# Optimization experiments

Measured on AMD Instinct MI355X. Metric: run time of the kernel, lower is better.

The kernel has to match this reference:

```python
import jax, jax.numpy as jnp
import numpy as np

QUERY_DIM = 768
KEY_DIM = 1024


def setup_inputs() -> dict:
    key = jax.random.key(0)
    ks = jax.random.split(key, 8)
    B, LQ, LK = 16, 2048, 2048
    s_q = 1.0 / np.sqrt(QUERY_DIM)
    s_k = 1.0 / np.sqrt(KEY_DIM)
    return {
        "query": jax.random.normal(ks[0], (B, LQ, QUERY_DIM), jnp.float32),
        "key": jax.random.normal(ks[1], (B, LK, KEY_DIM), jnp.float32),
        "Wq": jax.random.uniform(ks[2], (QUERY_DIM, KEY_DIM), jnp.float32, -s_q, s_q),
        "bq": jax.random.uniform(ks[3], (KEY_DIM,), jnp.float32, -s_q, s_q),
        "Wk": jax.random.uniform(ks[4], (KEY_DIM, KEY_DIM), jnp.float32, -s_k, s_k),
        "bk": jax.random.uniform(ks[5], (KEY_DIM,), jnp.float32, -s_k, s_k),
        "Wv": jax.random.uniform(ks[6], (KEY_DIM, KEY_DIM), jnp.float32, -s_k, s_k),
        "bv": jax.random.uniform(ks[7], (KEY_DIM,), jnp.float32, -s_k, s_k),
    }


def reference(query, key, Wq, bq, Wk, bk, Wv, bv):
    # Linear projections (single-head)
    q = jnp.einsum('bqd,dk->bqk', query, Wq) + bq  # [B, Lq, Dk]
    k = jnp.einsum('bsd,dk->bsk', key, Wk) + bk    # [B, Lk, Dk]
    v = jnp.einsum('bsd,dk->bsk', key, Wv) + bv    # [B, Lk, Dk]
    d_k = k.shape[-1]
    scores = jnp.einsum('bqk,bsk->bqs', q, k) / jnp.sqrt(jnp.asarray(d_k, q.dtype))
    weights = jax.nn.softmax(scores, axis=-1)      # [B, Lq, Lk]
    return jnp.einsum('bqs,bsk->bqk', weights, v)  # [B, Lq, Dk]
```

## Files before the change

kernel.cpp:

```cpp
#include <hip/hip_runtime.h>
#include <hip/hip_bf16.h>


typedef __attribute__((ext_vector_type(4))) float  f32x4;
typedef __attribute__((ext_vector_type(8))) __bf16 bf16x8;

#define BM 256
#define BN 256
#define BK 32

__device__ __forceinline__ void gload_lds16(const __bf16* g, __bf16* l) {
    __builtin_amdgcn_global_load_lds(
        (const __attribute__((address_space(1))) void*)g,
        (__attribute__((address_space(3))) void*)l, 16, 0, 0);
}

enum { MODE_PROJ = 0, MODE_PROJT = 1, MODE_SCORE = 2, MODE_PV = 3 };

#define MF(m_, a_)                                                              \
    acc[m_][0] = __builtin_amdgcn_mfma_f32_16x16x32_bf16(a_, b0, acc[m_][0], 0, 0, 0); \
    acc[m_][1] = __builtin_amdgcn_mfma_f32_16x16x32_bf16(a_, b1, acc[m_][1], 0, 0, 0); \
    acc[m_][2] = __builtin_amdgcn_mfma_f32_16x16x32_bf16(a_, b2, acc[m_][2], 0, 0, 0); \
    acc[m_][3] = __builtin_amdgcn_mfma_f32_16x16x32_bf16(a_, b3, acc[m_][3], 0, 0, 0);

#define TILE_STEP(CA_, CB_, SA_, SB_, DO_STAGE, VM_WAIT) do {                   \
    bf16x8 a0, a1, a2, a3, a4, a5, a6, a7, b0, b1, b2, b3;                      \
                                        \
    b0 = *(const bf16x8*)&CB_[raB];                                             \
    b1 = *(const bf16x8*)&CB_[raB + 512];                                       \
    b2 = *(const bf16x8*)&CB_[raB + 1024];                                      \
    b3 = *(const bf16x8*)&CB_[raB + 1536];                                      \
    a0 = *(const bf16x8*)&CA_[raA];                                             \
    a1 = *(const bf16x8*)&CA_[raA + 512];                                       \
    a2 = *(const bf16x8*)&CA_[raA + 1024];                                      \
    a3 = *(const bf16x8*)&CA_[raA + 1536];                                      \
    if (DO_STAGE) {                                                             \
        gload_lds16(ap0, &SA_[wA]);                                             \
        gload_lds16(ap1, &SA_[wA + 512]);                                       \
        ap0 += BK; ap1 += BK;                                                   \
    }                                                                           \
    __builtin_amdgcn_s_barrier();                                               \
    __builtin_amdgcn_s_setprio(1);                                              \
    MF(0, a0) MF(1, a1) MF(2, a2) MF(3, a3)                                     \
    __builtin_amdgcn_s_setprio(0);                                              \
    __builtin_amdgcn_s_barrier();                                               \
                        \
    a4 = *(const bf16x8*)&CA_[raA + 2048];                                      \
    a5 = *(const bf16x8*)&CA_[raA + 2560];                                      \
    a6 = *(const bf16x8*)&CA_[raA + 3072];                                      \
    a7 = *(const bf16x8*)&CA_[raA + 3584];                                      \
    if (DO_STAGE) {                                                             \
        gload_lds16(bp0, &SB_[wA]);                                             \
        gload_lds16(bp1, &SB_[wA + 512]);                                       \
        bp0 += BK; bp1 += BK;                                                   \
    }                                                                           \
    VM_WAIT;                                                                    \
    __builtin_amdgcn_s_barrier();                                               \
    __builtin_amdgcn_s_setprio(1);                                              \
    MF(4, a4) MF(5, a5) MF(6, a6) MF(7, a7)                                     \
    __builtin_amdgcn_s_setprio(0);                                              \
    __builtin_amdgcn_s_barrier();                                               \
} while (0)

template <int MODE>
__global__ __launch_bounds__(512, 2) void gemm256(
    const __bf16* __restrict__ Ag, const __bf16* __restrict__ Bg,
    const float* __restrict__ aux,
    float* __restrict__ rs,
    void* __restrict__ Cg,
    int K, int lda, int ldb, int ldc,
    long batchA, long batchB, long batchC, long batchRS)
{
    __shared__ __bf16 As0[BM * BK], As1[BM * BK], As2[BM * BK], As3[BM * BK];
    __shared__ __bf16 Bs0[BN * BK], Bs1[BN * BK], Bs2[BN * BK], Bs3[BN * BK];
    const int t    = threadIdx.x;
    const int lane = t & 63;
    const int w    = t >> 6;
    const int quad = lane >> 4;
    const int l15  = lane & 15;
    const int wm   = w >> 2, wn = w & 3;
    const int m0   = blockIdx.x * BM;
    const int n0   = blockIdx.y * BN;
    const int z    = blockIdx.z;

    const __bf16* A = Ag + (long)z * batchA;
    const __bf16* B = Bg + (long)z * batchB;

    const int srow = lane >> 2;
    const int sq   = ((lane & 3) ^ ((lane >> 3) & 3)) * 8;
    const __bf16* ap0 = A + (long)(m0 + w * 32 +      srow) * lda + sq;
    const __bf16* ap1 = A + (long)(m0 + w * 32 + 16 + srow) * lda + sq;
    const __bf16* bp0 = B + (long)(n0 + w * 32 +      srow) * ldb + sq;
    const __bf16* bp1 = B + (long)(n0 + w * 32 + 16 + srow) * ldb + sq;
    const int wA = w * 1024;

    const int swz = (quad ^ ((l15 >> 1) & 3)) * 8;
    const int raA = (wm * 128 + l15) * BK + swz;
    const int raB = (wn * 64  + l15) * BK + swz;

    f32x4 acc[8][4];
    #pragma unroll
    for (int i = 0; i < 8; ++i)
        #pragma unroll
        for (int j = 0; j < 4; ++j) acc[i][j] = (f32x4)(0.0f);

    const int NT = K / BK;

    gload_lds16(ap0, &As0[wA]); gload_lds16(ap1, &As0[wA + 512]);
    gload_lds16(bp0, &Bs0[wA]); gload_lds16(bp1, &Bs0[wA + 512]);
    ap0 += BK; ap1 += BK; bp0 += BK; bp1 += BK;
    gload_lds16(ap0, &As1[wA]); gload_lds16(ap1, &As1[wA + 512]);
    gload_lds16(bp0, &Bs1[wA]); gload_lds16(bp1, &Bs1[wA + 512]);
    ap0 += BK; ap1 += BK; bp0 += BK; bp1 += BK;
    gload_lds16(ap0, &As2[wA]); gload_lds16(ap1, &As2[wA + 512]);
    gload_lds16(bp0, &Bs2[wA]); gload_lds16(bp1, &Bs2[wA + 512]);
    ap0 += BK; ap1 += BK; bp0 += BK; bp1 += BK;
    asm volatile("s_waitcnt vmcnt(8)");
    __builtin_amdgcn_s_barrier();

    const int chunks = (NT - 4) >> 2;
    for (int c = 0; c < chunks; ++c) {
        TILE_STEP(As0, Bs0, As3, Bs3, 1, asm volatile("s_waitcnt vmcnt(8)"));
        TILE_STEP(As1, Bs1, As0, Bs0, 1, asm volatile("s_waitcnt vmcnt(8)"));
        TILE_STEP(As2, Bs2, As1, Bs1, 1, asm volatile("s_waitcnt vmcnt(8)"));
        TILE_STEP(As3, Bs3, As2, Bs2, 1, asm volatile("s_waitcnt vmcnt(8)"));
    }
    TILE_STEP(As0, Bs0, As3, Bs3, 1, asm volatile("s_waitcnt vmcnt(8)"));
    TILE_STEP(As1, Bs1, As0, Bs0, 0, asm volatile("s_waitcnt vmcnt(4)"));
    TILE_STEP(As2, Bs2, As0, Bs0, 0, asm volatile("s_waitcnt vmcnt(0)"));
    TILE_STEP(As3, Bs3, As0, Bs0, 0, ((void)0));

    const int rowbase = m0 + wm * 128;
    const int colbase = n0 + wn * 64;

    if constexpr (MODE == MODE_PROJ) {
        __bf16* C = (__bf16*)Cg;
        #pragma unroll
        for (int n = 0; n < 4; ++n) {
            const int col = colbase + n * 16 + l15;
            const float bv = aux[col];
            #pragma unroll
            for (int m = 0; m < 8; ++m)
                #pragma unroll
                for (int r = 0; r < 4; ++r) {
                    const int row = rowbase + m * 16 + quad * 4 + r;
                    C[(long)row * ldc + col] = (__bf16)(acc[m][n][r] + bv);
                }
        }
    } else if constexpr (MODE == MODE_PROJT) {
        __bf16* C = (__bf16*)Cg;
        #pragma unroll
        for (int m = 0; m < 8; ++m)
            #pragma unroll
            for (int r = 0; r < 4; ++r) {
                const int row = rowbase + m * 16 + quad * 4 + r;
                const float bv = aux[row];
                #pragma unroll
                for (int n = 0; n < 4; ++n) {
                    const int col = colbase + n * 16 + l15;
                    const long idx = (long)(col >> 11) * (1024L * 2048)
                                   + (long)row * 2048 + (col & 2047);
                    C[idx] = (__bf16)(acc[m][n][r] + bv);
                }
            }
    } else if constexpr (MODE == MODE_SCORE) {
        const float sc = 0.03125f * 1.44269504088896f;
        __bf16* C = (__bf16*)Cg + (long)z * batchC;
        float* rsz = rs + (long)z * batchRS;
        #pragma unroll
        for (int m = 0; m < 8; ++m) {
            float s[4] = {0.f, 0.f, 0.f, 0.f};
            #pragma unroll
            for (int n = 0; n < 4; ++n) {
                const int col = colbase + n * 16 + l15;
                #pragma unroll
                for (int r = 0; r < 4; ++r) {
                    const int row = rowbase + m * 16 + quad * 4 + r;
                    const float e = exp2f(acc[m][n][r] * sc);
                    C[(long)row * ldc + col] = (__bf16)e;
                    s[r] += e;
                }
            }
            #pragma unroll
            for (int r = 0; r < 4; ++r) {
                float v = s[r];
                v += __shfl_xor(v, 1);
                v += __shfl_xor(v, 2);
                v += __shfl_xor(v, 4);
                v += __shfl_xor(v, 8);
                if (l15 == 0)
                    atomicAdd(&rsz[rowbase + m * 16 + quad * 4 + r], v);
            }
        }
    } else {
        float* C = (float*)Cg + (long)z * batchC;
        const float* rsz = rs + (long)z * batchRS;
        #pragma unroll
        for (int m = 0; m < 8; ++m) {
            float inv[4];
            #pragma unroll
            for (int r = 0; r < 4; ++r)
                inv[r] = 1.0f / rsz[rowbase + m * 16 + quad * 4 + r];
            #pragma unroll
            for (int n = 0; n < 4; ++n) {
                const int col = colbase + n * 16 + l15;
                #pragma unroll
                for (int r = 0; r < 4; ++r) {
                    const int row = rowbase + m * 16 + quad * 4 + r;
                    C[(long)row * ldc + col] = acc[m][n][r] * inv[r];
                }
            }
        }
    }
}

__global__ __launch_bounds__(256) void conv_bf16(const float* __restrict__ in,
                                                 __bf16* __restrict__ out, long n8)
{
    const long stride = (long)gridDim.x * blockDim.x;
    for (long i = (long)blockIdx.x * blockDim.x + threadIdx.x; i < n8; i += stride) {
        const float4* p = (const float4*)(in + i * 8);
        const float4 a = p[0], b = p[1];
        bf16x8 o;
        o[0] = (__bf16)a.x; o[1] = (__bf16)a.y; o[2] = (__bf16)a.z; o[3] = (__bf16)a.w;
        o[4] = (__bf16)b.x; o[5] = (__bf16)b.y; o[6] = (__bf16)b.z; o[7] = (__bf16)b.w;
        *(bf16x8*)(out + i * 8) = o;
    }
}

__global__ __launch_bounds__(256) void transpose_w(const float* __restrict__ W,
                                                   __bf16* __restrict__ WT,
                                                   int K, int N)
{
    __shared__ float tile[32][33];
    const int n0 = blockIdx.x * 32, k0 = blockIdx.y * 32;
    const int c = threadIdx.x & 31, r4 = threadIdx.x >> 5;
    #pragma unroll
    for (int i = 0; i < 4; ++i) {
        const int r = r4 + i * 8;
        tile[r][c] = W[(long)(k0 + r) * N + n0 + c];
    }
    __syncthreads();
    #pragma unroll
    for (int i = 0; i < 4; ++i) {
        const int r = r4 + i * 8;
        WT[(long)(n0 + r) * K + k0 + c] = (__bf16)tile[c][r];
    }
}

extern "C" void kernel_launch(void* const* d_in, const int* in_sizes, int n_in,
                              void* d_out, int out_size, void* d_ws, size_t ws_size,
                              hipStream_t stream) {
    const float* query = (const float*)d_in[0];
    const float* key   = (const float*)d_in[1];
    const float* Wq    = (const float*)d_in[2];
    const float* bq    = (const float*)d_in[3];
    const float* Wk    = (const float*)d_in[4];
    const float* bk    = (const float*)d_in[5];
    const float* Wv    = (const float*)d_in[6];
    const float* bv    = (const float*)d_in[7];
    float* out = (float*)d_out;

    const int B = 16, Lq = 2048, Lk = 2048, Dq = 768, Dk = 1024;
    const long M = (long)B * Lq;

    char* base = (char*)d_ws;
    __bf16* P   = (__bf16*)base;
    __bf16* qa  = (__bf16*)base;
    __bf16* ka  = (__bf16*)(base + 50331648);
    __bf16* WqT = (__bf16*)(base + 117440512);
    __bf16* WkT = (__bf16*)(base + 119013376);
    __bf16* WvT = (__bf16*)(base + 121110528);
    char* p2 = base + 134217728;
    __bf16* q  = (__bf16*)p2;  p2 += M * Dk * 2;
    __bf16* k  = (__bf16*)p2;  p2 += M * Dk * 2;
    __bf16* vT = (__bf16*)p2;  p2 += M * Dk * 2;
    float* row_sum = (float*)p2; p2 += M * 4;
    if ((size_t)(p2 - base) > ws_size) return;

    dim3 blk(256);
    dim3 blk5(512);

    conv_bf16<<<512, blk, 0, stream>>>(query, qa, M * Dq / 8);
    conv_bf16<<<512, blk, 0, stream>>>(key,   ka, M * Dk / 8);
    transpose_w<<<dim3(Dk / 32, Dq / 32), blk, 0, stream>>>(Wq, WqT, Dq, Dk);
    transpose_w<<<dim3(Dk / 32, Dk / 32), blk, 0, stream>>>(Wk, WkT, Dk, Dk);
    transpose_w<<<dim3(Dk / 32, Dk / 32), blk, 0, stream>>>(Wv, WvT, Dk, Dk);
    hipMemsetAsync(row_sum, 0, M * 4, stream);

    gemm256<MODE_PROJ><<<dim3(M / BM, Dk / BN, 1), blk5, 0, stream>>>(
        qa, WqT, bq, nullptr, q, Dq, Dq, Dq, Dk, 0, 0, 0, 0);
    gemm256<MODE_PROJ><<<dim3(M / BM, Dk / BN, 1), blk5, 0, stream>>>(
        ka, WkT, bk, nullptr, k, Dk, Dk, Dk, Dk, 0, 0, 0, 0);
    gemm256<MODE_PROJT><<<dim3(Dk / BM, M / BN, 1), blk5, 0, stream>>>(
        WvT, ka, bv, nullptr, vT, Dk, Dk, Dk, 0, 0, 0, 0, 0);

    gemm256<MODE_SCORE><<<dim3(Lq / BM, Lk / BN, B), blk5, 0, stream>>>(
        q, k, nullptr, row_sum, P, Dk, Dk, Dk, Lk,
        (long)Lq * Dk, (long)Lk * Dk, (long)Lq * Lk, Lq);

    gemm256<MODE_PV><<<dim3(Lq / BM, Dk / BN, B), blk5, 0, stream>>>(
        P, vT, nullptr, row_sum, out, Lk, Lk, 2048, Dk,
        (long)Lq * Lk, 1024L * 2048, (long)Lq * Dk, Lq);
}
```

Measured before the change: 914.7 us.

## Replace direct global-to-LDS loads with register-staged double buffering

Global tiles are now loaded into registers one step ahead and written to LDS with ordinary vector stores, replacing the four-stage global_load_lds pipeline with a two-buffer LDS ping-pong. This cuts shared memory from four stages to two per operand, which could allow more resident blocks or lower LDS pressure. In exchange it costs extra VGPRs for the staged data and adds LDS write traffic and lgkmcnt waits inside the main loop, and it shortens the prefetch distance.

```diff
diff --git a/kernel.cpp b/kernel.cpp
--- a/kernel.cpp
+++ b/kernel.cpp
@@ -8,12 +8,6 @@
 #define BM 256
 #define BN 256
 #define BK 32
-
-__device__ __forceinline__ void gload_lds16(const __bf16* g, __bf16* l) {
-    __builtin_amdgcn_global_load_lds(
-        (const __attribute__((address_space(1))) void*)g,
-        (__attribute__((address_space(3))) void*)l, 16, 0, 0);
-}
 
 enum { MODE_PROJ = 0, MODE_PROJT = 1, MODE_SCORE = 2, MODE_PV = 3 };
 
@@ -23,9 +17,15 @@
     acc[m_][2] = __builtin_amdgcn_mfma_f32_16x16x32_bf16(a_, b2, acc[m_][2], 0, 0, 0); \
     acc[m_][3] = __builtin_amdgcn_mfma_f32_16x16x32_bf16(a_, b3, acc[m_][3], 0, 0, 0);
 
-#define TILE_STEP(CA_, CB_, SA_, SB_, DO_STAGE, VM_WAIT) do {                   \
+#define TILE_STEP(CA_, CB_, WA_, WB_, w0_, w1_, w2_, w3_,                       \
+                  l0_, l1_, l2_, l3_, DO_WRITE, DO_LOAD) do {                   \
     bf16x8 a0, a1, a2, a3, a4, a5, a6, a7, b0, b1, b2, b3;                      \
-                                        \
+     \
+    if (DO_LOAD) {                                                              \
+        l0_ = *(const bf16x8*)ap0; l1_ = *(const bf16x8*)ap1;                   \
+        l2_ = *(const bf16x8*)bp0; l3_ = *(const bf16x8*)bp1;                   \
+        ap0 += BK; ap1 += BK; bp0 += BK; bp1 += BK;                             \
+    }                                                                           \
     b0 = *(const bf16x8*)&CB_[raB];                                             \
     b1 = *(const bf16x8*)&CB_[raB + 512];                                       \
     b2 = *(const bf16x8*)&CB_[raB + 1024];                                      \
@@ -34,27 +34,23 @@
     a1 = *(const bf16x8*)&CA_[raA + 512];                                       \
     a2 = *(const bf16x8*)&CA_[raA + 1024];                                      \
     a3 = *(const bf16x8*)&CA_[raA + 1536];                                      \
-    if (DO_STAGE) {                                                             \
-        gload_lds16(ap0, &SA_[wA]);                                             \
-        gload_lds16(ap1, &SA_[wA + 512]);                                       \
-        ap0 += BK; ap1 += BK;                                                   \
+    if (DO_WRITE) {               \
+        *(bf16x8*)&WA_[wA + lane8]       = w0_;                                 \
+        *(bf16x8*)&WA_[wA + 512 + lane8] = w1_;                                 \
+        *(bf16x8*)&WB_[wA + lane8]       = w2_;                                 \
+        *(bf16x8*)&WB_[wA + 512 + lane8] = w3_;                                 \
     }                                                                           \
     __builtin_amdgcn_s_barrier();                                               \
     __builtin_amdgcn_s_setprio(1);                                              \
     MF(0, a0) MF(1, a1) MF(2, a2) MF(3, a3)                                     \
     __builtin_amdgcn_s_setprio(0);                                              \
+    if (DO_WRITE) asm volatile("s_waitcnt lgkmcnt(0)");     \
     __builtin_amdgcn_s_barrier();                                               \
-                        \
+                                                         \
     a4 = *(const bf16x8*)&CA_[raA + 2048];                                      \
     a5 = *(const bf16x8*)&CA_[raA + 2560];                                      \
     a6 = *(const bf16x8*)&CA_[raA + 3072];                                      \
     a7 = *(const bf16x8*)&CA_[raA + 3584];                                      \
-    if (DO_STAGE) {                                                             \
-        gload_lds16(bp0, &SB_[wA]);                                             \
-        gload_lds16(bp1, &SB_[wA + 512]);                                       \
-        bp0 += BK; bp1 += BK;                                                   \
-    }                                                                           \
-    VM_WAIT;                                                                    \
     __builtin_amdgcn_s_barrier();                                               \
     __builtin_amdgcn_s_setprio(1);                                              \
     MF(4, a4) MF(5, a5) MF(6, a6) MF(7, a7)                                     \
@@ -71,8 +67,8 @@
     int K, int lda, int ldb, int ldc,
     long batchA, long batchB, long batchC, long batchRS)
 {
-    __shared__ __bf16 As0[BM * BK], As1[BM * BK], As2[BM * BK], As3[BM * BK];
-    __shared__ __bf16 Bs0[BN * BK], Bs1[BN * BK], Bs2[BN * BK], Bs3[BN * BK];
+    __shared__ __bf16 As0[BM * BK], As1[BM * BK];
+    __shared__ __bf16 Bs0[BN * BK], Bs1[BN * BK];
     const int t    = threadIdx.x;
     const int lane = t & 63;
     const int w    = t >> 6;
@@ -92,7 +88,8 @@
     const __bf16* ap1 = A + (long)(m0 + w * 32 + 16 + srow) * lda + sq;
     const __bf16* bp0 = B + (long)(n0 + w * 32 +      srow) * ldb + sq;
     const __bf16* bp1 = B + (long)(n0 + w * 32 + 16 + srow) * ldb + sq;
-    const int wA = w * 1024;
+    const int wA    = w * 1024;
+    const int lane8 = lane * 8;
 
     const int swz = (quad ^ ((l15 >> 1) & 3)) * 8;
     const int raA = (wm * 128 + l15) * BK + swz;
@@ -106,29 +103,29 @@
 
     const int NT = K / BK;
 
-    gload_lds16(ap0, &As0[wA]); gload_lds16(ap1, &As0[wA + 512]);
-    gload_lds16(bp0, &Bs0[wA]); gload_lds16(bp1, &Bs0[wA + 512]);
-    ap0 += BK; ap1 += BK; bp0 += BK; bp1 += BK;
-    gload_lds16(ap0, &As1[wA]); gload_lds16(ap1, &As1[wA + 512]);
-    gload_lds16(bp0, &Bs1[wA]); gload_lds16(bp1, &Bs1[wA + 512]);
-    ap0 += BK; ap1 += BK; bp0 += BK; bp1 += BK;
-    gload_lds16(ap0, &As2[wA]); gload_lds16(ap1, &As2[wA + 512]);
-    gload_lds16(bp0, &Bs2[wA]); gload_lds16(bp1, &Bs2[wA + 512]);
-    ap0 += BK; ap1 += BK; bp0 += BK; bp1 += BK;
-    asm volatile("s_waitcnt vmcnt(8)");
-    __builtin_amdgcn_s_barrier();
-
-    const int chunks = (NT - 4) >> 2;
-    for (int c = 0; c < chunks; ++c) {
-        TILE_STEP(As0, Bs0, As3, Bs3, 1, asm volatile("s_waitcnt vmcnt(8)"));
-        TILE_STEP(As1, Bs1, As0, Bs0, 1, asm volatile("s_waitcnt vmcnt(8)"));
-        TILE_STEP(As2, Bs2, As1, Bs1, 1, asm volatile("s_waitcnt vmcnt(8)"));
-        TILE_STEP(As3, Bs3, As2, Bs2, 1, asm volatile("s_waitcnt vmcnt(8)"));
-    }
-    TILE_STEP(As0, Bs0, As3, Bs3, 1, asm volatile("s_waitcnt vmcnt(8)"));
-    TILE_STEP(As1, Bs1, As0, Bs0, 0, asm volatile("s_waitcnt vmcnt(4)"));
-    TILE_STEP(As2, Bs2, As0, Bs0, 0, asm volatile("s_waitcnt vmcnt(0)"));
-    TILE_STEP(As3, Bs3, As0, Bs0, 0, ((void)0));
+    bf16x8 q0, q1, q2, q3, r0, r1, r2, r3;
+
+    {
+        bf16x8 t0 = *(const bf16x8*)ap0, t1 = *(const bf16x8*)ap1;
+        bf16x8 t2 = *(const bf16x8*)bp0, t3 = *(const bf16x8*)bp1;
+        ap0 += BK; ap1 += BK; bp0 += BK; bp1 += BK;
+        r0 = *(const bf16x8*)ap0; r1 = *(const bf16x8*)ap1;
+        r2 = *(const bf16x8*)bp0; r3 = *(const bf16x8*)bp1;
+        ap0 += BK; ap1 += BK; bp0 += BK; bp1 += BK;
+        *(bf16x8*)&As0[wA + lane8]       = t0;
+        *(bf16x8*)&As0[wA + 512 + lane8] = t1;
+        *(bf16x8*)&Bs0[wA + lane8]       = t2;
+        *(bf16x8*)&Bs0[wA + 512 + lane8] = t3;
+        asm volatile("s_waitcnt lgkmcnt(0)");
+        __builtin_amdgcn_s_barrier();
+    }
+
+    for (int tt = 0; tt < NT - 2; tt += 2) {
+        TILE_STEP(As0, Bs0, As1, Bs1, r0, r1, r2, r3, q0, q1, q2, q3, 1, 1);
+        TILE_STEP(As1, Bs1, As0, Bs0, q0, q1, q2, q3, r0, r1, r2, r3, 1, 1);
+    }
+    TILE_STEP(As0, Bs0, As1, Bs1, r0, r1, r2, r3, q0, q1, q2, q3, 1, 0);
+    TILE_STEP(As1, Bs1, As0, Bs0, q0, q1, q2, q3, r0, r1, r2, r3, 0, 0);
 
     const int rowbase = m0 + wm * 128;
     const int colbase = n0 + wn * 64;
```

After: 887.4 us. 1.03x faster.
